# Kernel optimization log

Measured on AMD Instinct MI355X. Metric: run time of the kernel, lower is better.

The kernel has to match this reference:

```python
import jax, jax.numpy as jnp
import numpy as np

FP8_E4M3_MAX = 448.0

def setup_inputs() -> dict:
    key = jax.random.key(0)
    k1, k2, k3 = jax.random.split(key, 3)
    B, S, D_IN, D_OUT = 2, 4096, 2048, 8192
    x = jax.random.normal(k1, (B, S, D_IN), dtype=jnp.float32)
    # Xavier-uniform init for weight [out, in]
    limit = np.sqrt(6.0 / (D_IN + D_OUT)).astype(np.float32)
    weight = jax.random.uniform(k2, (D_OUT, D_IN), dtype=jnp.float32, minval=-limit, maxval=limit)
    bias = jax.random.normal(k3, (D_OUT,), dtype=jnp.float32) * 0.02
    return {"x": x, "weight": weight, "bias": bias}

def reference(x, weight, bias):
    # Dynamic amax-based scales (most_recent algo); treated as constants (torch uses .item())
    w_scale = jax.lax.stop_gradient(jnp.max(jnp.abs(weight)) / FP8_E4M3_MAX)
    x_scale = jax.lax.stop_gradient(jnp.max(jnp.abs(x)) / FP8_E4M3_MAX)
    # Quantize: divide by scale, cast (bf16 stands in for fp8 e4m3, as in the fallback branch)
    w_q = (weight / w_scale).astype(jnp.bfloat16)
    x_q = (x / x_scale).astype(jnp.bfloat16)
    # Matmul in quantized domain, then rescale
    out = jnp.einsum('bsd,od->bso', x_q, w_q)  # bf16 accumulate per fallback semantics
    out = out.astype(jnp.float32) * (w_scale * x_scale)
    out = out + bias
    return out.astype(x.dtype)
```

## Files before the change

kernel.cpp:

```cpp
#include <hip/hip_runtime.h>
#include <hip/hip_bf16.h>

#define M_DIM 8192
#define N_DIM 8192
#define K_DIM 2048
#define BM 128
#define BN 128
#define BK 32

typedef __attribute__((ext_vector_type(8))) short bf16x8;
typedef __attribute__((ext_vector_type(4))) float floatx4;

__device__ inline void gload_lds16(const void* g, void* l) {
  __builtin_amdgcn_global_load_lds(
      (const __attribute__((address_space(1))) unsigned int*)g,
      (__attribute__((address_space(3))) unsigned int*)l, 16, 0, 0);
}

__device__ inline short f2bf(float f) {
  __hip_bfloat16 h = __float2bfloat16(f);
  return *(short*)&h;
}

__device__ inline float round_bf16(float f) {
  __hip_bfloat16 h = __float2bfloat16(f);
  return __bfloat162float(h);
}

__global__ __launch_bounds__(256) void amax2_kernel(const float* __restrict__ x,
                                                    const float* __restrict__ w,
                                                    int n,
                                                    unsigned int* __restrict__ bits) {
  int b = blockIdx.x;
  const float* src;
  unsigned int* ob;
  if (b < 1024) { src = x; ob = bits + 0; } else { src = w; ob = bits + 1; b -= 1024; }
  int tid = threadIdx.x;
  int start = (b * 256 + tid) * 4;
  const int stride = 1024 * 256 * 4;
  float m = 0.0f;
  for (int i = start; i < n; i += stride) {
    float4 v = *(const float4*)(src + i);
    m = fmaxf(m, fmaxf(fmaxf(fabsf(v.x), fabsf(v.y)), fmaxf(fabsf(v.z), fabsf(v.w))));
  }
  for (int off = 32; off > 0; off >>= 1) m = fmaxf(m, __shfl_down(m, off));
  __shared__ float red[4];
  if ((tid & 63) == 0) red[tid >> 6] = m;
  __syncthreads();
  if (tid == 0) {
    m = fmaxf(fmaxf(red[0], red[1]), fmaxf(red[2], red[3]));
    atomicMax(ob, __float_as_uint(m));
  }
}

__global__ __launch_bounds__(256) void quant2_kernel(const float* __restrict__ x,
                                                     const float* __restrict__ w,
                                                     short* __restrict__ xq,
                                                     short* __restrict__ wq,
                                                     const unsigned int* __restrict__ bits) {
  int b = blockIdx.x;
  const float* src;
  short* dst;
  const unsigned int* ab;
  if (b < 8192) { src = x; dst = xq; ab = bits + 0; }
  else          { src = w; dst = wq; ab = bits + 1; b -= 8192; }
  float scale = __uint_as_float(*ab) / 448.0f;
  int idx = (b * 256 + threadIdx.x) * 8;
  float4 v0 = *(const float4*)(src + idx);
  float4 v1 = *(const float4*)(src + idx + 4);
  bf16x8 o;
  o[0] = f2bf(v0.x / scale);
  o[1] = f2bf(v0.y / scale);
  o[2] = f2bf(v0.z / scale);
  o[3] = f2bf(v0.w / scale);
  o[4] = f2bf(v1.x / scale);
  o[5] = f2bf(v1.y / scale);
  o[6] = f2bf(v1.z / scale);
  o[7] = f2bf(v1.w / scale);
  *(bf16x8*)(dst + idx) = o;
}

__global__ __launch_bounds__(256, 2) void gemm_kernel(
    const short* __restrict__ A,
    const short* __restrict__ B,
    const float* __restrict__ bias,
    const unsigned int* __restrict__ amax_bits,
    float* __restrict__ C) {
  __shared__ short As[BM * BK];
  __shared__ short Bs[BN * BK];

  const int tid = threadIdx.x;
  const int lane = tid & 63;
  const int waveId = tid >> 6;
  const int waveM = waveId >> 1;
  const int waveN = waveId & 1;
  const int m0 = blockIdx.y * BM;
  const int n0 = blockIdx.x * BN;

  const int r0 = tid >> 2;
  const int q0 = (tid & 3) ^ ((tid >> 3) & 3);
  const short* aSrc0 = A + (long)(m0 + r0) * K_DIM + q0 * 8;
  const short* aSrc1 = A + (long)(m0 + r0 + 64) * K_DIM + q0 * 8;
  const short* bSrc0 = B + (long)(n0 + r0) * K_DIM + q0 * 8;
  const short* bSrc1 = B + (long)(n0 + r0 + 64) * K_DIM + q0 * 8;
  short* aDst0 = As + tid * 8;
  short* aDst1 = As + (tid + 256) * 8;
  short* bDst0 = Bs + tid * 8;
  short* bDst1 = Bs + (tid + 256) * 8;

  floatx4 acc[4][4] = {};

  const int am = waveM * 64 + (lane & 15);
  const int bn = waveN * 64 + (lane & 15);
  const int ak = ((lane >> 4) ^ ((lane >> 1) & 3)) * 8;

  for (int kt = 0; kt < K_DIM / BK; ++kt) {
    const int ko = kt * BK;
    gload_lds16(aSrc0 + ko, aDst0);
    gload_lds16(aSrc1 + ko, aDst1);
    gload_lds16(bSrc0 + ko, bDst0);
    gload_lds16(bSrc1 + ko, bDst1);
    __syncthreads();

    bf16x8 af[4], bfr[4];
#pragma unroll
    for (int i = 0; i < 4; ++i)
      af[i] = *(const bf16x8*)(As + (am + i * 16) * BK + ak);
#pragma unroll
    for (int j = 0; j < 4; ++j)
      bfr[j] = *(const bf16x8*)(Bs + (bn + j * 16) * BK + ak);

#pragma unroll
    for (int i = 0; i < 4; ++i)
#pragma unroll
      for (int j = 0; j < 4; ++j)
        acc[i][j] = __builtin_amdgcn_mfma_f32_16x16x32_bf16(af[i], bfr[j], acc[i][j], 0, 0, 0);

    __syncthreads();
  }

  const float sx = __uint_as_float(amax_bits[0]) / 448.0f;
  const float sw = __uint_as_float(amax_bits[1]) / 448.0f;
  const float s = sx * sw;
  const int col = lane & 15;
  const int rq = (lane >> 4) * 4;
#pragma unroll
  for (int j = 0; j < 4; ++j) {
    const int n = n0 + waveN * 64 + j * 16 + col;
    const float bv = bias[n];
#pragma unroll
    for (int i = 0; i < 4; ++i) {
      const int mBase = m0 + waveM * 64 + i * 16 + rq;
#pragma unroll
      for (int r = 0; r < 4; ++r) {
        float v = round_bf16(acc[i][j][r]);
        C[(long)(mBase + r) * N_DIM + n] = v * s + bv;
      }
    }
  }
}

extern "C" void kernel_launch(void* const* d_in, const int* in_sizes, int n_in,
                              void* d_out, int out_size, void* d_ws, size_t ws_size,
                              hipStream_t stream) {
  const float* x = (const float*)d_in[0];
  const float* w = (const float*)d_in[1];
  const float* bias = (const float*)d_in[2];
  float* out = (float*)d_out;

  unsigned int* bits = (unsigned int*)d_ws;
  short* xq = (short*)((char*)d_ws + 256);
  short* wq = (short*)((char*)d_ws + 256 + (size_t)M_DIM * K_DIM * sizeof(short));

  hipMemsetAsync(d_ws, 0, 64, stream);

  amax2_kernel<<<2048, 256, 0, stream>>>(x, w, M_DIM * K_DIM, bits);
  quant2_kernel<<<16384, 256, 0, stream>>>(x, w, xq, wq, bits);
  gemm_kernel<<<dim3(N_DIM / BN, M_DIM / BM), 256, 0, stream>>>(xq, wq, bias, bits, out);
}
```

Measured before the change: 674.9 us.

## Rewrite GEMM with 256x256 tiles, triple-buffered LDS pipeline and block swizzle

```diff
diff --git a/kernel.cpp b/kernel.cpp
--- a/kernel.cpp
+++ b/kernel.cpp
@@ -4,14 +4,15 @@
 #define M_DIM 8192
 #define N_DIM 8192
 #define K_DIM 2048
-#define BM 128
-#define BN 128
+#define BM 256
+#define BN 256
 #define BK 32
+#define NT (K_DIM / BK)
 
 typedef __attribute__((ext_vector_type(8))) short bf16x8;
 typedef __attribute__((ext_vector_type(4))) float floatx4;
 
-__device__ inline void gload_lds16(const void* g, void* l) {
+__device__ __forceinline__ void gload_lds16(const void* g, void* l) {
   __builtin_amdgcn_global_load_lds(
       (const __attribute__((address_space(1))) unsigned int*)g,
       (__attribute__((address_space(3))) unsigned int*)l, 16, 0, 0);
@@ -80,64 +81,120 @@
   *(bf16x8*)(dst + idx) = o;
 }
 
-__global__ __launch_bounds__(256, 2) void gemm_kernel(
+
+template <int MODE>
+__device__ __forceinline__ void tile_body(
+    short* lds, int cur, int nxt, int t,
+    const short* aS0, const short* aS1, const short* bS0, const short* bS1,
+    int tid, int rA, int rB, int ak, floatx4 (&acc)[8][4]) {
+  short* sA = lds + cur * 16384;
+  short* sB = sA + 8192;
+  const int ko2 = (t + 2) * BK;
+
+  bf16x8 a0[4], bfr[4], a1[4];
+#pragma unroll
+  for (int i = 0; i < 4; ++i)
+    a0[i] = *(const bf16x8*)(sA + (rA + i * 16) * BK + ak);
+#pragma unroll
+  for (int j = 0; j < 4; ++j)
+    bfr[j] = *(const bf16x8*)(sB + (rB + j * 16) * BK + ak);
+  if constexpr (MODE == 0) {
+    short* d = lds + nxt * 16384;
+    gload_lds16(aS0 + ko2, d + tid * 8);
+    gload_lds16(aS1 + ko2, d + 4096 + tid * 8);
+  }
+  __builtin_amdgcn_s_barrier();
+  asm volatile("s_waitcnt lgkmcnt(0)" ::: "memory");
+  __builtin_amdgcn_s_setprio(1);
+#pragma unroll
+  for (int i = 0; i < 4; ++i)
+#pragma unroll
+    for (int j = 0; j < 4; ++j)
+      acc[i][j] = __builtin_amdgcn_mfma_f32_16x16x32_bf16(a0[i], bfr[j], acc[i][j], 0, 0, 0);
+  __builtin_amdgcn_s_setprio(0);
+  __builtin_amdgcn_s_barrier();
+
+#pragma unroll
+  for (int i = 0; i < 4; ++i)
+    a1[i] = *(const bf16x8*)(sA + (rA + 64 + i * 16) * BK + ak);
+  if constexpr (MODE == 0) {
+    short* d = lds + nxt * 16384 + 8192;
+    gload_lds16(bS0 + ko2, d + tid * 8);
+    gload_lds16(bS1 + ko2, d + 4096 + tid * 8);
+  }
+  __builtin_amdgcn_s_barrier();
+  asm volatile("s_waitcnt lgkmcnt(0)" ::: "memory");
+  __builtin_amdgcn_s_setprio(1);
+#pragma unroll
+  for (int i = 0; i < 4; ++i)
+#pragma unroll
+    for (int j = 0; j < 4; ++j)
+      acc[4 + i][j] = __builtin_amdgcn_mfma_f32_16x16x32_bf16(a1[i], bfr[j], acc[4 + i][j], 0, 0, 0);
+  __builtin_amdgcn_s_setprio(0);
+  if constexpr (MODE == 0)
+    asm volatile("s_waitcnt vmcnt(4)" ::: "memory");
+  else if constexpr (MODE == 1)
+    asm volatile("s_waitcnt vmcnt(0)" ::: "memory");
+  if constexpr (MODE != 2) __builtin_amdgcn_s_barrier();
+}
+
+__global__ __launch_bounds__(512, 2) void gemm_kernel(
     const short* __restrict__ A,
     const short* __restrict__ B,
     const float* __restrict__ bias,
     const unsigned int* __restrict__ amax_bits,
     float* __restrict__ C) {
-  __shared__ short As[BM * BK];
-  __shared__ short Bs[BN * BK];
+  __shared__ short lds[3 * 16384];
 
   const int tid = threadIdx.x;
   const int lane = tid & 63;
   const int waveId = tid >> 6;
-  const int waveM = waveId >> 1;
-  const int waveN = waveId & 1;
-  const int m0 = blockIdx.y * BM;
-  const int n0 = blockIdx.x * BN;
+  const int waveM = waveId >> 2;
+  const int waveN = waveId & 3;
+
+  int bid = blockIdx.y * 32 + blockIdx.x;
+  bid = (bid & 7) * 128 + (bid >> 3);
+  const int m0 = (bid >> 5) * BM;
+  const int n0 = (bid & 31) * BN;
 
   const int r0 = tid >> 2;
   const int q0 = (tid & 3) ^ ((tid >> 3) & 3);
-  const short* aSrc0 = A + (long)(m0 + r0) * K_DIM + q0 * 8;
-  const short* aSrc1 = A + (long)(m0 + r0 + 64) * K_DIM + q0 * 8;
-  const short* bSrc0 = B + (long)(n0 + r0) * K_DIM + q0 * 8;
-  const short* bSrc1 = B + (long)(n0 + r0 + 64) * K_DIM + q0 * 8;
-  short* aDst0 = As + tid * 8;
-  short* aDst1 = As + (tid + 256) * 8;
-  short* bDst0 = Bs + tid * 8;
-  short* bDst1 = Bs + (tid + 256) * 8;
-
-  floatx4 acc[4][4] = {};
-
-  const int am = waveM * 64 + (lane & 15);
-  const int bn = waveN * 64 + (lane & 15);
+  const short* aS0 = A + (long)(m0 + r0) * K_DIM + q0 * 8;
+  const short* aS1 = aS0 + (long)128 * K_DIM;
+  const short* bS0 = B + (long)(n0 + r0) * K_DIM + q0 * 8;
+  const short* bS1 = bS0 + (long)128 * K_DIM;
+
+  const int rA = waveM * 128 + (lane & 15);
+  const int rB = waveN * 64 + (lane & 15);
   const int ak = ((lane >> 4) ^ ((lane >> 1) & 3)) * 8;
 
-  for (int kt = 0; kt < K_DIM / BK; ++kt) {
-    const int ko = kt * BK;
-    gload_lds16(aSrc0 + ko, aDst0);
-    gload_lds16(aSrc1 + ko, aDst1);
-    gload_lds16(bSrc0 + ko, bDst0);
-    gload_lds16(bSrc1 + ko, bDst1);
-    __syncthreads();
-
-    bf16x8 af[4], bfr[4];
-#pragma unroll
-    for (int i = 0; i < 4; ++i)
-      af[i] = *(const bf16x8*)(As + (am + i * 16) * BK + ak);
-#pragma unroll
-    for (int j = 0; j < 4; ++j)
-      bfr[j] = *(const bf16x8*)(Bs + (bn + j * 16) * BK + ak);
-
-#pragma unroll
-    for (int i = 0; i < 4; ++i)
-#pragma unroll
-      for (int j = 0; j < 4; ++j)
-        acc[i][j] = __builtin_amdgcn_mfma_f32_16x16x32_bf16(af[i], bfr[j], acc[i][j], 0, 0, 0);
-
-    __syncthreads();
-  }
+  floatx4 acc[8][4] = {};
+
+  {
+    short* d0 = lds;
+    gload_lds16(aS0, d0 + tid * 8);
+    gload_lds16(aS1, d0 + 4096 + tid * 8);
+    gload_lds16(bS0, d0 + 8192 + tid * 8);
+    gload_lds16(bS1, d0 + 8192 + 4096 + tid * 8);
+    short* d1 = lds + 16384;
+    gload_lds16(aS0 + BK, d1 + tid * 8);
+    gload_lds16(aS1 + BK, d1 + 4096 + tid * 8);
+    gload_lds16(bS0 + BK, d1 + 8192 + tid * 8);
+    gload_lds16(bS1 + BK, d1 + 8192 + 4096 + tid * 8);
+  }
+  asm volatile("s_waitcnt vmcnt(4)" ::: "memory");
+  __builtin_amdgcn_s_barrier();
+
+#pragma unroll 1
+  for (int tt = 0; tt < 60; tt += 3) {
+    tile_body<0>(lds, 0, 2, tt,     aS0, aS1, bS0, bS1, tid, rA, rB, ak, acc);
+    tile_body<0>(lds, 1, 0, tt + 1, aS0, aS1, bS0, bS1, tid, rA, rB, ak, acc);
+    tile_body<0>(lds, 2, 1, tt + 2, aS0, aS1, bS0, bS1, tid, rA, rB, ak, acc);
+  }
+  tile_body<0>(lds, 0, 2, 60, aS0, aS1, bS0, bS1, tid, rA, rB, ak, acc);
+  tile_body<0>(lds, 1, 0, 61, aS0, aS1, bS0, bS1, tid, rA, rB, ak, acc);
+  tile_body<1>(lds, 2, 0, 62, aS0, aS1, bS0, bS1, tid, rA, rB, ak, acc);
+  tile_body<2>(lds, 0, 0, 63, aS0, aS1, bS0, bS1, tid, rA, rB, ak, acc);
 
   const float sx = __uint_as_float(amax_bits[0]) / 448.0f;
   const float sw = __uint_as_float(amax_bits[1]) / 448.0f;
@@ -149,12 +206,12 @@
     const int n = n0 + waveN * 64 + j * 16 + col;
     const float bv = bias[n];
 #pragma unroll
-    for (int i = 0; i < 4; ++i) {
-      const int mBase = m0 + waveM * 64 + i * 16 + rq;
+    for (int fi = 0; fi < 8; ++fi) {
+      const int mBase = m0 + waveM * 128 + fi * 16 + rq;
 #pragma unroll
       for (int r = 0; r < 4; ++r) {
-        float v = round_bf16(acc[i][j][r]);
-        C[(long)(mBase + r) * N_DIM + n] = v * s + bv;
+        float v = round_bf16(acc[fi][j][r]);
+        __builtin_nontemporal_store(v * s + bv, &C[(long)(mBase + r) * N_DIM + n]);
       }
     }
   }
@@ -176,5 +233,5 @@
 
   amax2_kernel<<<2048, 256, 0, stream>>>(x, w, M_DIM * K_DIM, bits);
   quant2_kernel<<<16384, 256, 0, stream>>>(x, w, xq, wq, bits);
-  gemm_kernel<<<dim3(N_DIM / BN, M_DIM / BM), 256, 0, stream>>>(xq, wq, bias, bits, out);
-}
+  gemm_kernel<<<dim3(N_DIM / BN, M_DIM / BM), 512, 0, stream>>>(xq, wq, bias, bits, out);
+}
```

New measurement: 605.7 us. 1.11x faster.
